# Performance work log

Measured on AMD Instinct MI355X. Metric: run time of the kernel, lower is better.

The kernel has to match this reference:

```python
import jax, jax.numpy as jnp
import numpy as np

NUM_HEADS = 16
LORA_SCALE = 32.0 / 8.0  # alpha / rank
ROPE_BASE = 10000.0


def make_sincos(seq_len, dim):
    # theta[t, j] = t / base**( (2j)/dim ), shapes (T, dim//2)
    pos = jnp.arange(seq_len, dtype=jnp.float32)
    i = jnp.arange(0, dim, 2, dtype=jnp.float32) / dim
    theta = pos[:, None] / (ROPE_BASE ** i[None, :])
    return jnp.sin(theta), jnp.cos(theta)


def apply_rope(x, sin, cos):
    # x: (B, h, T, d) with interleaved even/odd rotation pairs
    x_even = x[..., 0::2]
    x_odd = x[..., 1::2]
    rot_even = x_even * cos - x_odd * sin
    rot_odd = x_even * sin + x_odd * cos
    return jnp.stack([rot_even, rot_odd], axis=-1).reshape(x.shape)


def setup_inputs() -> dict:
    key = jax.random.key(0)
    ks = jax.random.split(key, 9)
    B, T, D, R = 4, 2048, 1024, 8
    s = 1.0 / np.sqrt(D)
    return {
        "query": jax.random.normal(ks[0], (B, T, D), dtype=jnp.float32),
        "wq": jax.random.normal(ks[1], (D, D), dtype=jnp.float32) * s,
        "wk": jax.random.normal(ks[2], (D, D), dtype=jnp.float32) * s,
        "wv": jax.random.normal(ks[3], (D, D), dtype=jnp.float32) * s,
        "wo": jax.random.normal(ks[4], (D, D), dtype=jnp.float32) * s,
        "Aq": jax.random.normal(ks[5], (D, R), dtype=jnp.float32) * s,
        "Bq": jax.random.normal(ks[6], (R, D), dtype=jnp.float32) * 0.01,
        "Av": jax.random.normal(ks[7], (D, R), dtype=jnp.float32) * s,
        "Bv": jax.random.normal(ks[8], (R, D), dtype=jnp.float32) * 0.01,
    }


def reference(query, wq, wk, wv, wo, Aq, Bq, Av, Bv):
    B, T, D = query.shape
    H = NUM_HEADS
    dh = D // H

    # fused base + LoRA projections (self-attention: key=value=query)
    q = query @ wq + ((query @ Aq) @ Bq) * LORA_SCALE
    k = query @ wk
    v = query @ wv + ((query @ Av) @ Bv) * LORA_SCALE

    def split(x):  # (B,T,D) -> (B,H,T,dh)
        return x.reshape(B, T, H, dh).transpose(0, 2, 1, 3)

    q, k, v = split(q), split(k), split(v)

    sin, cos = make_sincos(T, dh)
    q = apply_rope(q, sin, cos)
    k = apply_rope(k, sin, cos)

    scores = jnp.einsum("bhqd,bhkd->bhqk", q, k) / jnp.sqrt(jnp.float32(dh))
    causal = jnp.triu(jnp.ones((T, T), dtype=bool), k=1)  # mask == 1 -> blocked
    scores = jnp.where(causal[None, None], jnp.float32(-1e9), scores)
    attn = jax.nn.softmax(scores, axis=-1)  # dropout p=0 -> identity

    out = jnp.einsum("bhqk,bhkd->bhqd", attn, v)
    out = out.transpose(0, 2, 1, 3).reshape(B, T, D)
    return out @ wo
```

## Files before the change

kernel.cpp:

```cpp
#include <hip/hip_runtime.h>
#include <cstdint>

#define B_  4
#define T_  2048
#define D_  1024
#define H_  16
#define DH_ 64
#define R_  8
#define M_  (B_*T_)
#define LORA_SCALE 4.0f

typedef __attribute__((ext_vector_type(8))) short    bf16x8;
typedef __attribute__((ext_vector_type(4))) short    bf16x4;
typedef __attribute__((ext_vector_type(4))) float    f32x4;
typedef __attribute__((ext_vector_type(4))) uint32_t u32x4;

__device__ inline uint16_t f2b(float f) {
    uint32_t x = __float_as_uint(f);
    return (uint16_t)((x + 0x7fffu + ((x >> 16) & 1u)) >> 16);
}
__device__ inline float b2f(uint16_t u) { return __uint_as_float(((uint32_t)u) << 16); }

__device__ __forceinline__ uint32_t cvtpk(float lo, float hi) {
    uint32_t r;
    asm("v_cvt_pk_bf16_f32 %0, %1, %2" : "=v"(r) : "v"(lo), "v"(hi));
    return r;
}
__device__ __forceinline__ float max3f(float a, float b, float c) {
    float r;
    asm("v_max3_f32 %0, %1, %2, %3" : "=v"(r) : "v"(a), "v"(b), "v"(c));
    return r;
}

__device__ __forceinline__ void gld_lds16(const uint16_t* g, uint16_t* l) {
    __builtin_amdgcn_global_load_lds(
        (const __attribute__((address_space(1))) void*)g,
        (__attribute__((address_space(3))) void*)l, 16, 0, 0);
}

__global__ void cast_x_kernel(const float* __restrict__ x, uint16_t* __restrict__ out) {
    int g = blockIdx.x * 256 + threadIdx.x;
    const float4* xv = (const float4*)x;
    float4 a = xv[2 * g], b = xv[2 * g + 1];
    union { u32x4 v; uint16_t s[8]; } u;
    u.s[0] = f2b(a.x); u.s[1] = f2b(a.y); u.s[2] = f2b(a.z); u.s[3] = f2b(a.w);
    u.s[4] = f2b(b.x); u.s[5] = f2b(b.y); u.s[6] = f2b(b.z); u.s[7] = f2b(b.w);
    ((u32x4*)out)[g] = u.v;
}

__global__ void make_wt_kernel(const float* __restrict__ wq, const float* __restrict__ wk,
                               const float* __restrict__ wv, const float* __restrict__ wo,
                               const float* __restrict__ Aq, const float* __restrict__ Bq,
                               const float* __restrict__ Av, const float* __restrict__ Bv,
                               uint16_t* __restrict__ Wt) {
    __shared__ float tile[64][65];
    int mat = blockIdx.z;
    int n0 = blockIdx.x * 64, k0 = blockIdx.y * 64;
    const float* W  = (mat == 0) ? wq : (mat == 1) ? wk : (mat == 2) ? wv : wo;
    const float* Ap = (mat == 0) ? Aq : (mat == 2) ? Av : nullptr;
    const float* Bp = (mat == 0) ? Bq : (mat == 2) ? Bv : nullptr;
    int t = threadIdx.x;
    int r = t >> 2, c0 = (t & 3) * 16;
    int k = k0 + r;
    #pragma unroll
    for (int j = 0; j < 16; j++) {
        int n = n0 + c0 + j;
        float v = W[(size_t)k * D_ + n];
        if (Ap) {
            float acc = 0.f;
            #pragma unroll
            for (int rr = 0; rr < R_; rr++) acc += Ap[k * R_ + rr] * Bp[rr * D_ + n];
            v += LORA_SCALE * acc;
        }
        tile[r][c0 + j] = v;
    }
    __syncthreads();
    int nl = t >> 2, ks = (t & 3) * 16;
    union { uint16_t s[16]; u32x4 v[2]; } uo;
    #pragma unroll
    for (int j = 0; j < 16; j++) uo.s[j] = f2b(tile[ks + j][nl]);
    uint16_t* dst = Wt + (size_t)mat * D_ * D_ + (size_t)(n0 + nl) * D_ + k0 + ks;
    *(u32x4*)&dst[0] = uo.v[0];
    *(u32x4*)&dst[8] = uo.v[1];
}

template <bool OUT_F32>
__global__ __launch_bounds__(256)
void gemm_bt_kernel(const uint16_t* __restrict__ A, const uint16_t* __restrict__ Bt,
                    uint16_t* __restrict__ Cb, float* __restrict__ Cf,
                    int Mdim, int Ndim, int Kdim) {
    __shared__ uint16_t At[128 * 32];
    __shared__ uint16_t Bs[128 * 32];
    int tid = threadIdx.x;
    int wave = tid >> 6, lane = tid & 63, quad = lane >> 4, l15 = lane & 15;
    int rowBase = blockIdx.y * 128, colBase = blockIdx.x * 128;
    int wRow = (wave >> 1) * 64, wCol = (wave & 1) * 64;
    int srow0 = tid >> 2, sseg0 = (tid & 3) * 8;
    int srow1 = (tid + 256) >> 2;
    f32x4 acc[4][4] = {};
    for (int kb = 0; kb < Kdim; kb += 32) {
        gld_lds16(&A [(size_t)(rowBase + srow0) * Kdim + kb + sseg0], &At[srow0 * 32 + sseg0]);
        gld_lds16(&A [(size_t)(rowBase + srow1) * Kdim + kb + sseg0], &At[srow1 * 32 + sseg0]);
        gld_lds16(&Bt[(size_t)(colBase + srow0) * Kdim + kb + sseg0], &Bs[srow0 * 32 + sseg0]);
        gld_lds16(&Bt[(size_t)(colBase + srow1) * Kdim + kb + sseg0], &Bs[srow1 * 32 + sseg0]);
        __syncthreads();
        bf16x8 af[4], bfr[4];
        #pragma unroll
        for (int m = 0; m < 4; m++) af[m]  = *(const bf16x8*)&At[(wRow + m * 16 + l15) * 32 + quad * 8];
        #pragma unroll
        for (int n = 0; n < 4; n++) bfr[n] = *(const bf16x8*)&Bs[(wCol + n * 16 + l15) * 32 + quad * 8];
        #pragma unroll
        for (int m = 0; m < 4; m++)
            #pragma unroll
            for (int n = 0; n < 4; n++)
                acc[m][n] = __builtin_amdgcn_mfma_f32_16x16x32_bf16(af[m], bfr[n], acc[m][n], 0, 0, 0);
        __syncthreads();
    }
    #pragma unroll
    for (int m = 0; m < 4; m++) {
        int row = rowBase + wRow + m * 16 + quad * 4;
        #pragma unroll
        for (int n = 0; n < 4; n++) {
            int col = colBase + wCol + n * 16 + l15;
            #pragma unroll
            for (int r = 0; r < 4; r++) {
                float v = acc[m][n][r];
                if (OUT_F32) Cf[(size_t)(row + r) * Ndim + col] = v;
                else         Cb[(size_t)(row + r) * Ndim + col] = f2b(v);
            }
        }
    }
}

__global__ void rope_kernel(const uint16_t* __restrict__ qkv,
                            uint16_t* __restrict__ Qr, uint16_t* __restrict__ Kr) {
    int g = blockIdx.x * 256 + threadIdx.x;
    int i  = g & 31;
    int t  = (g >> 5) & (T_ - 1);
    int bh = g >> 16;
    int h = bh & 15, b = bh >> 4;
    size_t rowoff = ((size_t)(b * T_ + t)) * 3072 + h * 64 + 2 * i;
    uint32_t qp = *(const uint32_t*)&qkv[rowoff];
    uint32_t kp = *(const uint32_t*)&qkv[rowoff + 1024];
    float qe = b2f((uint16_t)qp), qo = b2f((uint16_t)(qp >> 16));
    float ke = b2f((uint16_t)kp), ko = b2f((uint16_t)(kp >> 16));
    float inv = exp2f(-(float)i * (13.2877123795494f / 32.f));
    float th = (float)t * inv;
    float s = sinf(th), c = cosf(th);
    const float SC = 0.125f * 1.44269504089f;
    uint32_t qw = (uint32_t)f2b((qe * c - qo * s) * SC)
                | ((uint32_t)f2b((qe * s + qo * c) * SC) << 16);
    uint32_t kw = (uint32_t)f2b(ke * c - ko * s) | ((uint32_t)f2b(ke * s + ko * c) << 16);
    size_t o = ((size_t)bh * T_ + t) * 64 + 2 * i;
    *(uint32_t*)&Qr[o] = qw;
    int d = 2 * i;
    size_t kidx = ((size_t)bh * T_ + t) * 64 + ((((d >> 3) ^ (t & 7)) << 3) | (d & 7));
    *(uint32_t*)&Kr[kidx] = kw;
}

__global__ void vtrans_kernel(const uint16_t* __restrict__ qkv, uint16_t* __restrict__ Vt) {
    __shared__ uint16_t tile[32][72];
    int bh = blockIdx.y, t0 = blockIdx.x * 32;
    int b = bh >> 4, h = bh & 15;
    int tid = threadIdx.x;
    int r = tid >> 3, c8 = (tid & 7) * 8;
    *(u32x4*)&tile[r][c8] =
        *(const u32x4*)&qkv[((size_t)(b * T_ + t0 + r)) * 3072 + 2048 + h * 64 + c8];
    __syncthreads();
    int d = tid >> 2, t8 = (tid & 3) * 8;
    union { uint16_t s[8]; u32x4 v; } uu;
    #pragma unroll
    for (int j = 0; j < 8; j++) uu.s[j] = tile[t8 + j][d];
    int tt = t0 + t8;
    int c  = (tt & 127) >> 3;
    int phys = (c & 8) | ((c ^ (d & 7)) & 7);
    size_t vidx = (size_t)bh * 64 * T_ + (size_t)(tt >> 7) * 8192 + d * 128 + phys * 8;
    *(u32x4*)&Vt[vidx] = uu.v;
}

#define PSTR 136

__device__ __forceinline__ f32x4 mfma16(bf16x8 a, bf16x8 b, f32x4 c) {
    return __builtin_amdgcn_mfma_f32_16x16x32_bf16(a, b, c, 0, 0, 0);
}

template <bool MASKED>
__device__ __forceinline__ void attn_chunk_sw(
    const uint16_t* __restrict__ Kst, const uint16_t* __restrict__ Vst,
    uint16_t* __restrict__ Pw, int nact, int base_kmq,
    bf16x8 aQ0, bf16x8 aQ1, int l15, int quad,
    f32x4 (&Oacc)[4], float& mrow, float& lrow)
{
    int lx = l15 & 7;
    f32x4 sacc[8];
    #pragma unroll
    for (int n = 0; n < 8; n++) {
        if (MASKED && n >= nact) continue;
        int rowK = (n * 16 + l15) * 64;
        bf16x8 kv0 = *(const bf16x8*)&Kst[rowK + ((quad ^ lx) << 3)];
        bf16x8 kv1 = *(const bf16x8*)&Kst[rowK + (((quad + 4) ^ lx) << 3)];
        f32x4 s = {};
        s = mfma16(kv0, aQ0, s);
        s = mfma16(kv1, aQ1, s);
        sacc[n] = s;
    }
    float mx = -1e30f;
    #pragma unroll
    for (int n = 0; n < 8; n++) {
        if (MASKED && n >= nact) continue;
        if (MASKED) {
            #pragma unroll
            for (int r = 0; r < 4; r++) {
                int kmq = base_kmq + n * 16 + quad * 4 + r;
                if (kmq > 0) sacc[n][r] = -1e30f;
            }
        }
        float t = max3f(sacc[n][0], sacc[n][1], sacc[n][2]);
        mx = max3f(mx, t, sacc[n][3]);
    }
    mx = fmaxf(mx, __shfl_xor(mx, 16, 64));
    mx = fmaxf(mx, __shfl_xor(mx, 32, 64));
    if (!__all(mx <= mrow + 8.f)) {
        float mnew = fmaxf(mrow, mx);
        float alpha = exp2f(mrow - mnew);
        #pragma unroll
        for (int m = 0; m < 4; m++)
            #pragma unroll
            for (int r = 0; r < 4; r++) Oacc[m][r] *= alpha;
        lrow *= alpha;
        mrow = mnew;
    }
    float sum = 0.f;
    #pragma unroll
    for (int n = 0; n < 8; n++) {
        if (MASKED && n >= nact) continue;
        #pragma unroll
        for (int r = 0; r < 4; r++) {
            float e = exp2f(sacc[n][r] - mrow);
            sacc[n][r] = e;
            sum += e;
        }
    }
    sum += __shfl_xor(sum, 16, 64);
    sum += __shfl_xor(sum, 32, 64);
    lrow += sum;
    #pragma unroll
    for (int n = 0; n < 8; n++) {
        if (MASKED && n >= nact) continue;
        uint2 pk;
        pk.x = cvtpk(sacc[n][0], sacc[n][1]);
        pk.y = cvtpk(sacc[n][2], sacc[n][3]);
        *(uint2*)&Pw[l15 * PSTR + n * 16 + quad * 4] = pk;
    }
    if (MASKED && (nact & 1)) {
        uint2 z; z.x = 0u; z.y = 0u;
        *(uint2*)&Pw[l15 * PSTR + nact * 16 + quad * 4] = z;
    }
    int ssact = MASKED ? ((nact + 1) >> 1) : 4;
    #pragma unroll
    for (int ss = 0; ss < 4; ss++) {
        if (MASKED && ss >= ssact) continue;
        bf16x8 bP = *(const bf16x8*)&Pw[l15 * PSTR + ss * 32 + quad * 8];
        int cl = ss * 4 + quad;
        int phys = (cl & 8) | ((cl ^ lx) & 7);
        #pragma unroll
        for (int m = 0; m < 4; m++) {
            bf16x8 aV = *(const bf16x8*)&Vst[(m * 16 + l15) * 128 + (phys << 3)];
            Oacc[m] = mfma16(aV, bP, Oacc[m]);
        }
    }
}

__global__ __launch_bounds__(256, 3)
void attn_kernel(const uint16_t* __restrict__ Qr, const uint16_t* __restrict__ Kr,
                 const uint16_t* __restrict__ Vt, uint16_t* __restrict__ Obuf) {
    __shared__ uint16_t KLDS[128 * 64];
    __shared__ uint16_t VLDS[64 * 128];
    __shared__ uint16_t Pl[4][16 * PSTR];
    int id  = blockIdx.x;
    int xcd = id & 7, grp = id >> 3;
    int bh  = xcd * 8 + (grp & 7);
    int qx  = grp >> 3;
    int b = bh >> 4, h = bh & 15;
    int tid = threadIdx.x, wave = tid >> 6, lane = tid & 63, quad = lane >> 4, l15 = lane & 15;
    const uint16_t* Qbase = Qr + (size_t)bh * T_ * 64;
    const uint16_t* Kbase = Kr + (size_t)bh * T_ * 64;
    const uint16_t* Vbase = Vt + (size_t)bh * 64 * T_;
    uint16_t* Pw = &Pl[wave][0];
    #pragma unroll
    for (int pass = 0; pass < 2; pass++) {
        int qt = pass ? (31 - qx) : qx;
        int q0w = qt * 64 + wave * 16;
        bf16x8 aQ0 = *(const bf16x8*)&Qbase[(size_t)(q0w + l15) * 64 + quad * 8];
        bf16x8 aQ1 = *(const bf16x8*)&Qbase[(size_t)(q0w + l15) * 64 + 32 + quad * 8];
        f32x4 Oacc[4] = {};
        float mrow = -1e30f, lrow = 0.f;
        int nch = (qt >> 1) + 1;
        int klim = q0w + 15;
        for (int c = 0; c < nch; c++) {
            int k0 = c * 128;
            __syncthreads();
            const uint16_t* gK = Kbase + (size_t)k0 * 64;
            const uint16_t* gV = Vbase + (size_t)k0 * 64;
            #pragma unroll
            for (int j = 0; j < 4; j++) {
                gld_lds16(gK + (tid + j * 256) * 8, &KLDS[(tid + j * 256) * 8]);
                gld_lds16(gV + (tid + j * 256) * 8, &VLDS[(tid + j * 256) * 8]);
            }
            __syncthreads();
            if (c == nch - 1) {
                int nact = ((klim - k0) >> 4) + 1;
                attn_chunk_sw<true>(KLDS, VLDS, Pw, nact, k0 - q0w - l15,
                                    aQ0, aQ1, l15, quad, Oacc, mrow, lrow);
            } else {
                attn_chunk_sw<false>(KLDS, VLDS, Pw, 8, 0,
                                     aQ0, aQ1, l15, quad, Oacc, mrow, lrow);
            }
        }
        float invl = 1.0f / lrow;
        float* Ow = (float*)Pw;
        #pragma unroll
        for (int m = 0; m < 4; m++) {
            f32x4 o;
            #pragma unroll
            for (int r = 0; r < 4; r++) o[r] = Oacc[m][r] * invl;
            *(f32x4*)&Ow[l15 * 68 + m * 16 + quad * 4] = o;
        }
        int orow = lane >> 2, ocol = (lane & 3) * 16;
        #pragma unroll
        for (int jj = 0; jj < 4; jj++) {
            f32x4 ov = *(const f32x4*)&Ow[orow * 68 + ocol + jj * 4];
            uint2 ob;
            ob.x = cvtpk(ov[0], ov[1]);
            ob.y = cvtpk(ov[2], ov[3]);
            *(uint2*)&Obuf[((size_t)(b * T_ + qt * 64 + wave * 16 + orow)) * D_
                            + h * 64 + ocol + jj * 4] = ob;
        }
    }
}

extern "C" void kernel_launch(void* const* d_in, const int* in_sizes, int n_in,
                              void* d_out, int out_size, void* d_ws, size_t ws_size,
                              hipStream_t stream) {
    const float* query = (const float*)d_in[0];
    const float* wq = (const float*)d_in[1];
    const float* wk = (const float*)d_in[2];
    const float* wv = (const float*)d_in[3];
    const float* wo = (const float*)d_in[4];
    const float* Aq = (const float*)d_in[5];
    const float* Bq = (const float*)d_in[6];
    const float* Av = (const float*)d_in[7];
    const float* Bv = (const float*)d_in[8];
    float* out = (float*)d_out;

    const size_t MB = 1ull << 20;
    if (ws_size < 120 * MB) return;
    char* ws = (char*)d_ws;
    uint16_t* Xbf = (uint16_t*)(ws);
    uint16_t* Wt  = (uint16_t*)(ws + 16 * MB);
    uint16_t* qkv = (uint16_t*)(ws + 24 * MB);
    uint16_t* Qr  = (uint16_t*)(ws + 72 * MB);
    uint16_t* Kr  = (uint16_t*)(ws + 88 * MB);
    uint16_t* Vt  = (uint16_t*)(ws + 104 * MB);
    uint16_t* Obuf = qkv;

    cast_x_kernel<<<4096, 256, 0, stream>>>(query, Xbf);
    make_wt_kernel<<<dim3(16, 16, 4), 256, 0, stream>>>(wq, wk, wv, wo, Aq, Bq, Av, Bv, Wt);
    gemm_bt_kernel<false><<<dim3(3072 / 128, M_ / 128), 256, 0, stream>>>(
        Xbf, Wt, qkv, nullptr, M_, 3072, D_);
    rope_kernel<<<16384, 256, 0, stream>>>(qkv, Qr, Kr);
    vtrans_kernel<<<dim3(T_ / 32, B_ * H_), 256, 0, stream>>>(qkv, Vt);
    attn_kernel<<<1024, 256, 0, stream>>>(Qr, Kr, Vt, Obuf);
    gemm_bt_kernel<true><<<dim3(D_ / 128, M_ / 128), 256, 0, stream>>>(
        Obuf, Wt + 3ull * D_ * D_, nullptr, out, M_, D_, D_);
}
```

Measured before the change: 328.4 us.

## Shrink attention KV chunks to 64 and drop paired q-tile passes for occupancy

Reduces the attention key/value chunk from 128 to 64 keys, which halves the LDS tiles and score registers, and raises launch bounds to 6 blocks per CU. The two-pass pairing of short and long causal query tiles is removed in favour of one query tile per block, with 2048 blocks scheduled longest-first. The V transpose layout is changed to 64-key blocks, and the output is written straight from registers instead of through an LDS staging step. In exchange, each block loops over more chunks and hits twice as many barriers, and the uncoalesced direct output stores and the loss of pairwise load balancing may cost time.

```diff
diff --git a/kernel.cpp b/kernel.cpp
--- a/kernel.cpp
+++ b/kernel.cpp
@@ -172,13 +172,13 @@
     #pragma unroll
     for (int j = 0; j < 8; j++) uu.s[j] = tile[t8 + j][d];
     int tt = t0 + t8;
-    int c  = (tt & 127) >> 3;
-    int phys = (c & 8) | ((c ^ (d & 7)) & 7);
-    size_t vidx = (size_t)bh * 64 * T_ + (size_t)(tt >> 7) * 8192 + d * 128 + phys * 8;
+    int c  = (tt & 63) >> 3;
+    int phys = (c ^ (d & 7)) & 7;
+    size_t vidx = (size_t)bh * 64 * T_ + (size_t)(tt >> 6) * 4096 + d * 64 + phys * 8;
     *(u32x4*)&Vt[vidx] = uu.v;
 }
 
-#define PSTR 136
+#define PSTR 72
 
 __device__ __forceinline__ f32x4 mfma16(bf16x8 a, bf16x8 b, f32x4 c) {
     return __builtin_amdgcn_mfma_f32_16x16x32_bf16(a, b, c, 0, 0, 0);
@@ -192,9 +192,13 @@
     f32x4 (&Oacc)[4], float& mrow, float& lrow)
 {
     int lx = l15 & 7;
-    f32x4 sacc[8];
-    #pragma unroll
-    for (int n = 0; n < 8; n++) {
+    f32x4 sacc[4];
+    if (MASKED) {
+        #pragma unroll
+        for (int n = 0; n < 4; n++) sacc[n] = f32x4{0.f, 0.f, 0.f, 0.f};
+    }
+    #pragma unroll
+    for (int n = 0; n < 4; n++) {
         if (MASKED && n >= nact) continue;
         int rowK = (n * 16 + l15) * 64;
         bf16x8 kv0 = *(const bf16x8*)&Kst[rowK + ((quad ^ lx) << 3)];
@@ -206,7 +210,7 @@
     }
     float mx = -1e30f;
     #pragma unroll
-    for (int n = 0; n < 8; n++) {
+    for (int n = 0; n < 4; n++) {
         if (MASKED && n >= nact) continue;
         if (MASKED) {
             #pragma unroll
@@ -232,7 +236,7 @@
     }
     float sum = 0.f;
     #pragma unroll
-    for (int n = 0; n < 8; n++) {
+    for (int n = 0; n < 4; n++) {
         if (MASKED && n >= nact) continue;
         #pragma unroll
         for (int r = 0; r < 4; r++) {
@@ -245,7 +249,7 @@
     sum += __shfl_xor(sum, 32, 64);
     lrow += sum;
     #pragma unroll
-    for (int n = 0; n < 8; n++) {
+    for (int n = 0; n < 4; n++) {
         if (MASKED && n >= nact) continue;
         uint2 pk;
         pk.x = cvtpk(sacc[n][0], sacc[n][1]);
@@ -256,86 +260,72 @@
         uint2 z; z.x = 0u; z.y = 0u;
         *(uint2*)&Pw[l15 * PSTR + nact * 16 + quad * 4] = z;
     }
-    int ssact = MASKED ? ((nact + 1) >> 1) : 4;
-    #pragma unroll
-    for (int ss = 0; ss < 4; ss++) {
+    int ssact = MASKED ? ((nact + 1) >> 1) : 2;
+    #pragma unroll
+    for (int ss = 0; ss < 2; ss++) {
         if (MASKED && ss >= ssact) continue;
         bf16x8 bP = *(const bf16x8*)&Pw[l15 * PSTR + ss * 32 + quad * 8];
         int cl = ss * 4 + quad;
-        int phys = (cl & 8) | ((cl ^ lx) & 7);
+        int phys = (cl ^ lx) & 7;
         #pragma unroll
         for (int m = 0; m < 4; m++) {
-            bf16x8 aV = *(const bf16x8*)&Vst[(m * 16 + l15) * 128 + (phys << 3)];
+            bf16x8 aV = *(const bf16x8*)&Vst[(m * 16 + l15) * 64 + (phys << 3)];
             Oacc[m] = mfma16(aV, bP, Oacc[m]);
         }
     }
 }
 
-__global__ __launch_bounds__(256, 3)
+__global__ __launch_bounds__(256, 6)
 void attn_kernel(const uint16_t* __restrict__ Qr, const uint16_t* __restrict__ Kr,
                  const uint16_t* __restrict__ Vt, uint16_t* __restrict__ Obuf) {
-    __shared__ uint16_t KLDS[128 * 64];
-    __shared__ uint16_t VLDS[64 * 128];
+    __shared__ uint16_t KLDS[64 * 64];
+    __shared__ uint16_t VLDS[64 * 64];
     __shared__ uint16_t Pl[4][16 * PSTR];
     int id  = blockIdx.x;
     int xcd = id & 7, grp = id >> 3;
     int bh  = xcd * 8 + (grp & 7);
-    int qx  = grp >> 3;
+    int qt  = 31 - (grp >> 3);
     int b = bh >> 4, h = bh & 15;
     int tid = threadIdx.x, wave = tid >> 6, lane = tid & 63, quad = lane >> 4, l15 = lane & 15;
     const uint16_t* Qbase = Qr + (size_t)bh * T_ * 64;
     const uint16_t* Kbase = Kr + (size_t)bh * T_ * 64;
     const uint16_t* Vbase = Vt + (size_t)bh * 64 * T_;
     uint16_t* Pw = &Pl[wave][0];
-    #pragma unroll
-    for (int pass = 0; pass < 2; pass++) {
-        int qt = pass ? (31 - qx) : qx;
-        int q0w = qt * 64 + wave * 16;
-        bf16x8 aQ0 = *(const bf16x8*)&Qbase[(size_t)(q0w + l15) * 64 + quad * 8];
-        bf16x8 aQ1 = *(const bf16x8*)&Qbase[(size_t)(q0w + l15) * 64 + 32 + quad * 8];
-        f32x4 Oacc[4] = {};
-        float mrow = -1e30f, lrow = 0.f;
-        int nch = (qt >> 1) + 1;
-        int klim = q0w + 15;
-        for (int c = 0; c < nch; c++) {
-            int k0 = c * 128;
-            __syncthreads();
-            const uint16_t* gK = Kbase + (size_t)k0 * 64;
-            const uint16_t* gV = Vbase + (size_t)k0 * 64;
-            #pragma unroll
-            for (int j = 0; j < 4; j++) {
-                gld_lds16(gK + (tid + j * 256) * 8, &KLDS[(tid + j * 256) * 8]);
-                gld_lds16(gV + (tid + j * 256) * 8, &VLDS[(tid + j * 256) * 8]);
-            }
-            __syncthreads();
-            if (c == nch - 1) {
-                int nact = ((klim - k0) >> 4) + 1;
-                attn_chunk_sw<true>(KLDS, VLDS, Pw, nact, k0 - q0w - l15,
-                                    aQ0, aQ1, l15, quad, Oacc, mrow, lrow);
-            } else {
-                attn_chunk_sw<false>(KLDS, VLDS, Pw, 8, 0,
-                                     aQ0, aQ1, l15, quad, Oacc, mrow, lrow);
-            }
-        }
-        float invl = 1.0f / lrow;
-        float* Ow = (float*)Pw;
-        #pragma unroll
-        for (int m = 0; m < 4; m++) {
-            f32x4 o;
-            #pragma unroll
-            for (int r = 0; r < 4; r++) o[r] = Oacc[m][r] * invl;
-            *(f32x4*)&Ow[l15 * 68 + m * 16 + quad * 4] = o;
-        }
-        int orow = lane >> 2, ocol = (lane & 3) * 16;
-        #pragma unroll
-        for (int jj = 0; jj < 4; jj++) {
-            f32x4 ov = *(const f32x4*)&Ow[orow * 68 + ocol + jj * 4];
-            uint2 ob;
-            ob.x = cvtpk(ov[0], ov[1]);
-            ob.y = cvtpk(ov[2], ov[3]);
-            *(uint2*)&Obuf[((size_t)(b * T_ + qt * 64 + wave * 16 + orow)) * D_
-                            + h * 64 + ocol + jj * 4] = ob;
-        }
+    int q0w = qt * 64 + wave * 16;
+    bf16x8 aQ0 = *(const bf16x8*)&Qbase[(size_t)(q0w + l15) * 64 + quad * 8];
+    bf16x8 aQ1 = *(const bf16x8*)&Qbase[(size_t)(q0w + l15) * 64 + 32 + quad * 8];
+    f32x4 Oacc[4] = {};
+    float mrow = -1e30f, lrow = 0.f;
+    int nch = qt + 1;
+    int klim = q0w + 15;
+    int idx0 = tid, idx1 = tid + 256;
+    for (int c = 0; c < nch; c++) {
+        int k0 = c * 64;
+        __syncthreads();
+        const uint16_t* gK = Kbase + (size_t)k0 * 64;
+        const uint16_t* gV = Vbase + (size_t)(k0 >> 6) * 4096;
+        gld_lds16(gK + idx0 * 8, &KLDS[idx0 * 8]);
+        gld_lds16(gK + idx1 * 8, &KLDS[idx1 * 8]);
+        gld_lds16(gV + idx0 * 8, &VLDS[idx0 * 8]);
+        gld_lds16(gV + idx1 * 8, &VLDS[idx1 * 8]);
+        __syncthreads();
+        if (c == nch - 1) {
+            int nact = ((klim - k0) >> 4) + 1;
+            attn_chunk_sw<true>(KLDS, VLDS, Pw, nact, k0 - q0w - l15,
+                                aQ0, aQ1, l15, quad, Oacc, mrow, lrow);
+        } else {
+            attn_chunk_sw<false>(KLDS, VLDS, Pw, 4, 0,
+                                 aQ0, aQ1, l15, quad, Oacc, mrow, lrow);
+        }
+    }
+    float invl = 1.0f / lrow;
+    size_t obase = ((size_t)(b * T_ + q0w + l15)) * D_ + h * 64;
+    #pragma unroll
+    for (int m = 0; m < 4; m++) {
+        uint2 ob;
+        ob.x = cvtpk(Oacc[m][0] * invl, Oacc[m][1] * invl);
+        ob.y = cvtpk(Oacc[m][2] * invl, Oacc[m][3] * invl);
+        *(uint2*)&Obuf[obase + m * 16 + quad * 4] = ob;
     }
 }
 
@@ -370,7 +360,7 @@
         Xbf, Wt, qkv, nullptr, M_, 3072, D_);
     rope_kernel<<<16384, 256, 0, stream>>>(qkv, Qr, Kr);
     vtrans_kernel<<<dim3(T_ / 32, B_ * H_), 256, 0, stream>>>(qkv, Vt);
-    attn_kernel<<<1024, 256, 0, stream>>>(Qr, Kr, Vt, Obuf);
+    attn_kernel<<<2048, 256, 0, stream>>>(Qr, Kr, Vt, Obuf);
     gemm_bt_kernel<true><<<dim3(D_ / 128, M_ / 128), 256, 0, stream>>>(
         Obuf, Wt + 3ull * D_ * D_, nullptr, out, M_, D_, D_);
 }
```

New measurement: 310.5 us. -5.4%, faster.
